# Kernel optimization log

Measured on AMD Instinct MI355X. Metric: run time of the kernel, lower is better.

## Reference

```python
import jax, jax.numpy as jnp
import numpy as np

N_SRC = 100000
N_DST = 100000
N_EDGES = 1600000
IN_FEATS = 256
HEADS = 4
D_OUT = 64
NEG_SLOPE = 0.2


def setup_inputs() -> dict:
    key = jax.random.key(0)
    ks = jax.random.split(key, 7)
    return {
        "feat_src": jax.random.normal(ks[0], (N_SRC, IN_FEATS), dtype=jnp.float32),
        "feat_dst": jax.random.normal(ks[1], (N_DST, IN_FEATS), dtype=jnp.float32),
        "edge_src": jax.random.randint(ks[2], (N_EDGES,), 0, N_SRC, dtype=jnp.int32),
        "edge_dst": jax.random.randint(ks[3], (N_EDGES,), 0, N_DST, dtype=jnp.int32),
        "W": jax.random.normal(ks[4], (IN_FEATS, HEADS * D_OUT), dtype=jnp.float32) * 0.06,
        "attn_l": jax.random.normal(ks[5], (HEADS, D_OUT), dtype=jnp.float32) * 0.1,
        "attn_r": jax.random.normal(ks[6], (HEADS, D_OUT), dtype=jnp.float32) * 0.1,
    }


def reference(feat_src, feat_dst, edge_src, edge_dst, W, attn_l, attn_r):
    # fc projection (no bias), reshape to [N, H, D]
    fsrc = (feat_src @ W).reshape(-1, HEADS, D_OUT)
    fdst = (feat_dst @ W).reshape(-1, HEADS, D_OUT)
    # per-node attention logits: el [N_src, H], er [N_dst, H]
    el = jnp.einsum('nhd,hd->nh', fsrc, attn_l)
    er = jnp.einsum('nhd,hd->nh', fdst, attn_r)
    # per-edge logit = leaky_relu(el[src] + er[dst]); original uses raw exp (no max-sub)
    e = el[edge_src] + er[edge_dst]                          # [E, H]
    e = jnp.where(e >= 0, e, NEG_SLOPE * e)
    s = jnp.exp(e)                                           # [E, H]
    # edge softmax denominator: segment sum over dst nodes
    out_sum = jax.ops.segment_sum(s, edge_dst, num_segments=N_DST)  # [N_dst, H]
    a = s / out_sum[edge_dst]                                # [E, H]
    # weighted neighbor aggregation: m = ft[src] * a, summed per dst
    m = fsrc[edge_src] * a[:, :, None]                       # [E, H, D]
    rst = jax.ops.segment_sum(m, edge_dst, num_segments=N_DST)      # [N_dst, H, D]
    return rst
```

## Files before the change

kernel.cpp:

```cpp
#include <hip/hip_runtime.h>
#include <hip/hip_bf16.h>
#include <math.h>

#define N_SRC   100000
#define N_DST   100000
#define N_EDGES 1600000
#define IN_F    256
#define HEADS   4
#define D_OUT   64
#define NHD     256
#define NEG_SLOPE 0.2f

typedef __attribute__((ext_vector_type(8))) short          bf16x8;
typedef __attribute__((ext_vector_type(8))) unsigned short u16x8;
typedef __attribute__((ext_vector_type(4))) float          f32x4;

__device__ inline void split_bf16(float x, unsigned short& h, unsigned short& l) {
    unsigned u = __float_as_uint(x);
    unsigned uh = u + (0x7fffu + ((u >> 16) & 1u));
    h = (unsigned short)(uh >> 16);
    float hf = __uint_as_float(uh & 0xffff0000u);
    float r = x - hf;
    unsigned ur = __float_as_uint(r);
    l = (unsigned short)((ur + (0x7fffu + ((ur >> 16) & 1u))) >> 16);
}

__global__ void k_wr(const float* __restrict__ W, const float* __restrict__ ar,
                     float* __restrict__ wr) {
    __shared__ float a[NHD];
    int t = threadIdx.x;
    a[t] = ar[t];
    __syncthreads();
    float s[HEADS] = {0.f, 0.f, 0.f, 0.f};
    for (int h = 0; h < HEADS; ++h) {
        float acc = 0.f;
        #pragma unroll 8
        for (int d = 0; d < D_OUT; ++d)
            acc += W[t * NHD + h * D_OUT + d] * a[h * D_OUT + d];
        s[h] = acc;
    }
    *(float4*)&wr[t * 4] = make_float4(s[0], s[1], s[2], s[3]);
}

__global__ void k_wcast(const float* __restrict__ W,
                        unsigned short* __restrict__ Wht,
                        unsigned short* __restrict__ Wlt) {
    int n = blockIdx.x;
    int k = threadIdx.x;
    float x = W[k * NHD + n];
    unsigned short h, l;
    split_bf16(x, h, l);
    Wht[n * IN_F + k] = h;
    Wlt[n * IN_F + k] = l;
}

__global__ __launch_bounds__(256) void k_er(const float* __restrict__ fdst,
                                            const float* __restrict__ wr,
                                            float* __restrict__ er) {
    __shared__ float4 wrs[256];
    int t = threadIdx.x;
    wrs[t] = ((const float4*)wr)[t];
    __syncthreads();
    int node = blockIdx.x * 4 + (t >> 6);
    int lane = t & 63;
    float4 f = *(const float4*)&fdst[(size_t)node * IN_F + lane * 4];
    float4 w0 = wrs[lane * 4 + 0], w1 = wrs[lane * 4 + 1];
    float4 w2 = wrs[lane * 4 + 2], w3 = wrs[lane * 4 + 3];
    float px = f.x * w0.x + f.y * w1.x + f.z * w2.x + f.w * w3.x;
    float py = f.x * w0.y + f.y * w1.y + f.z * w2.y + f.w * w3.y;
    float pz = f.x * w0.z + f.y * w1.z + f.z * w2.z + f.w * w3.z;
    float pw = f.x * w0.w + f.y * w1.w + f.z * w2.w + f.w * w3.w;
    #pragma unroll
    for (int m = 1; m < 64; m <<= 1) {
        px += __shfl_xor(px, m);
        py += __shfl_xor(py, m);
        pz += __shfl_xor(pz, m);
        pw += __shfl_xor(pw, m);
    }
    if (lane == 0)
        *(float4*)&er[node * 4] = make_float4(px, py, pz, pw);
}

#define GBM 128
#define GBK 32
__global__ __launch_bounds__(512, 2) void k_gemm_mfma(
        const float* __restrict__ A, const unsigned short* __restrict__ Bht,
        const unsigned short* __restrict__ Blt, const float* __restrict__ al_g,
        float* __restrict__ C, float* __restrict__ el) {
    __shared__ __align__(16) unsigned short Ah[GBM][GBK], Al[GBM][GBK];
    __shared__ __align__(16) unsigned short Bh[NHD][GBK], Bl[NHD][GBK];
    const int t = threadIdx.x;
    const int m0 = blockIdx.x * GBM;
    const int wid = t >> 6, lane = t & 63;
    const int wm = wid >> 2, wn = wid & 3;
    const int fr = lane & 15, fq = lane >> 4;
    const int kb = fq * 8;

    f32x4 acc[4][4];
    #pragma unroll
    for (int m = 0; m < 4; ++m)
        #pragma unroll
        for (int n = 0; n < 4; ++n)
            acc[m][n] = (f32x4){0.f, 0.f, 0.f, 0.f};

    const int ar = t >> 2, ac = (t & 3) * 8;
    const bool avalid = (m0 + ar) < N_SRC;
    const float* aptr = A + (size_t)(m0 + ar) * IN_F + ac;
    const int bn = t >> 1, bk = (t & 1) * 16;

    for (int k0 = 0; k0 < IN_F; k0 += GBK) {
        float4 v0 = make_float4(0.f, 0.f, 0.f, 0.f), v1 = v0;
        if (avalid) {
            v0 = *(const float4*)(aptr + k0);
            v1 = *(const float4*)(aptr + k0 + 4);
        }
        u16x8 bh0 = *(const u16x8*)(Bht + (size_t)bn * IN_F + k0 + bk);
        u16x8 bh1 = *(const u16x8*)(Bht + (size_t)bn * IN_F + k0 + bk + 8);
        u16x8 bl0 = *(const u16x8*)(Blt + (size_t)bn * IN_F + k0 + bk);
        u16x8 bl1 = *(const u16x8*)(Blt + (size_t)bn * IN_F + k0 + bk + 8);
        float xs[8] = {v0.x, v0.y, v0.z, v0.w, v1.x, v1.y, v1.z, v1.w};
        u16x8 hv, lv;
        #pragma unroll
        for (int j = 0; j < 8; ++j) {
            unsigned short hh, ll;
            split_bf16(xs[j], hh, ll);
            hv[j] = hh; lv[j] = ll;
        }
        __syncthreads();
        *(u16x8*)&Ah[ar][ac] = hv;
        *(u16x8*)&Al[ar][ac] = lv;
        *(u16x8*)&Bh[bn][bk]     = bh0;
        *(u16x8*)&Bh[bn][bk + 8] = bh1;
        *(u16x8*)&Bl[bn][bk]     = bl0;
        *(u16x8*)&Bl[bn][bk + 8] = bl1;
        __syncthreads();
        bf16x8 afh[4], afl[4], bfh[4], bfl[4];
        #pragma unroll
        for (int m = 0; m < 4; ++m) {
            afh[m] = *(const bf16x8*)&Ah[wm * 64 + m * 16 + fr][kb];
            afl[m] = *(const bf16x8*)&Al[wm * 64 + m * 16 + fr][kb];
        }
        #pragma unroll
        for (int n = 0; n < 4; ++n) {
            bfh[n] = *(const bf16x8*)&Bh[wn * 64 + n * 16 + fr][kb];
            bfl[n] = *(const bf16x8*)&Bl[wn * 64 + n * 16 + fr][kb];
        }
        #pragma unroll
        for (int m = 0; m < 4; ++m)
            #pragma unroll
            for (int n = 0; n < 4; ++n) {
                acc[m][n] = __builtin_amdgcn_mfma_f32_16x16x32_bf16(afh[m], bfh[n], acc[m][n], 0, 0, 0);
                acc[m][n] = __builtin_amdgcn_mfma_f32_16x16x32_bf16(afh[m], bfl[n], acc[m][n], 0, 0, 0);
                acc[m][n] = __builtin_amdgcn_mfma_f32_16x16x32_bf16(afl[m], bfh[n], acc[m][n], 0, 0, 0);
            }
    }

    float alw[4];
    #pragma unroll
    for (int n = 0; n < 4; ++n) alw[n] = al_g[wn * 64 + n * 16 + fr];
    #pragma unroll
    for (int m = 0; m < 4; ++m) {
        int rbase = m0 + wm * 64 + m * 16 + fq * 4;
        float elp[4] = {0.f, 0.f, 0.f, 0.f};
        #pragma unroll
        for (int n = 0; n < 4; ++n) {
            f32x4 a = acc[m][n];
            int col = wn * 64 + n * 16 + fr;
            float w = alw[n];
            elp[0] += a[0] * w; elp[1] += a[1] * w;
            elp[2] += a[2] * w; elp[3] += a[3] * w;
            #pragma unroll
            for (int j = 0; j < 4; ++j)
                if (rbase + j < N_SRC)
                    C[(size_t)(rbase + j) * NHD + col] = a[j];
        }
        #pragma unroll
        for (int j = 0; j < 4; ++j) {
            float s = elp[j];
            s += __shfl_xor(s, 1); s += __shfl_xor(s, 2);
            s += __shfl_xor(s, 4); s += __shfl_xor(s, 8);
            if (fr == 0 && rbase + j < N_SRC)
                el[(rbase + j) * HEADS + wn] = s;
        }
    }
}

__global__ void k_hist(const int* __restrict__ edst, int* __restrict__ deg) {
    int e = blockIdx.x * 256 + threadIdx.x;
    if (e < N_EDGES) atomicAdd(&deg[edst[e]], 1);
}

#define SCAN_B 1024
__global__ __launch_bounds__(SCAN_B) void k_scanA(const int* __restrict__ deg,
                                                  int* __restrict__ off,
                                                  int* __restrict__ bsum) {
    int t = threadIdx.x, b = blockIdx.x;
    int i = b * SCAN_B + t;
    int v = (i < N_DST) ? deg[i] : 0;
    int incl = v;
    int lane = t & 63, w = t >> 6;
    #pragma unroll
    for (int d = 1; d < 64; d <<= 1) {
        int u = __shfl_up(incl, d);
        if (lane >= d) incl += u;
    }
    __shared__ int ws[16];
    if (lane == 63) ws[w] = incl;
    __syncthreads();
    if (t == 0) {
        int run = 0;
        for (int j = 0; j < 16; ++j) { int x = ws[j]; ws[j] = run; run += x; }
        bsum[b] = run;
    }
    __syncthreads();
    if (i < N_DST) off[i] = incl - v + ws[w];
}

__global__ void k_scanB(int* __restrict__ bsum, int nb) {
    if (threadIdx.x == 0 && blockIdx.x == 0) {
        int run = 0;
        for (int j = 0; j < nb; ++j) { int x = bsum[j]; bsum[j] = run; run += x; }
    }
}

__global__ __launch_bounds__(SCAN_B) void k_scanC(int* __restrict__ off,
                                                  const int* __restrict__ bsum) {
    int t = threadIdx.x, b = blockIdx.x;
    int i = b * SCAN_B + t;
    if (i < N_DST) off[i] += bsum[b];
    if (i == 0) off[N_DST] = N_EDGES;
}

__global__ void k_scatter(const int* __restrict__ esrc, const int* __restrict__ edst,
                          const float* __restrict__ el, const float* __restrict__ er,
                          const int* __restrict__ off, int* __restrict__ cursor,
                          int* __restrict__ ssrc, float4* __restrict__ ss) {
    int e = blockIdx.x * 256 + threadIdx.x;
    if (e >= N_EDGES) return;
    int src = esrc[e], dst = edst[e];
    float4 l4 = *(const float4*)&el[src * 4];
    float4 r4 = *(const float4*)&er[dst * 4];
    float ex = l4.x + r4.x, ey = l4.y + r4.y, ez = l4.z + r4.z, ew = l4.w + r4.w;
    ex = (ex >= 0.f) ? ex : NEG_SLOPE * ex;
    ey = (ey >= 0.f) ? ey : NEG_SLOPE * ey;
    ez = (ez >= 0.f) ? ez : NEG_SLOPE * ez;
    ew = (ew >= 0.f) ? ew : NEG_SLOPE * ew;
    float4 s = make_float4(expf(ex), expf(ey), expf(ez), expf(ew));
    int pos = off[dst] + atomicAdd(&cursor[dst], 1);
    ssrc[pos] = src;
    ss[pos] = s;
}

__global__ __launch_bounds__(256) void k_agg(const int* __restrict__ off,
                                             const int* __restrict__ ssrc,
                                             const float* __restrict__ ss,
                                             const float* __restrict__ fsrc,
                                             float* __restrict__ out) {
    int b = blockIdx.x;
    int t = threadIdx.x;
    int s0 = off[b], s1 = off[b + 1];
    __shared__ float inv_den[HEADS];
    if (t < 64) {
        int h = t & 3;
        float p = 0.f;
        for (int i = s0 + (t >> 2); i < s1; i += 16)
            p += ss[(size_t)i * 4 + h];
        #pragma unroll
        for (int m = 4; m < 64; m <<= 1) p += __shfl_xor(p, m);
        if (t < 4) inv_den[t] = (p > 0.f) ? (1.0f / p) : 0.f;
    }
    __syncthreads();
    int h = t >> 6;
    float idh = inv_den[h];
    float acc = 0.f;
    int i = s0;
    int n4 = s0 + ((s1 - s0) & ~3);
    for (; i < n4; i += 4) {
        int sA = ssrc[i + 0], sB = ssrc[i + 1];
        int sC = ssrc[i + 2], sD = ssrc[i + 3];
        float aA = ss[(size_t)(i + 0) * 4 + h];
        float aB = ss[(size_t)(i + 1) * 4 + h];
        float aC = ss[(size_t)(i + 2) * 4 + h];
        float aD = ss[(size_t)(i + 3) * 4 + h];
        float fA = fsrc[(size_t)sA * NHD + t];
        float fB = fsrc[(size_t)sB * NHD + t];
        float fC = fsrc[(size_t)sC * NHD + t];
        float fD = fsrc[(size_t)sD * NHD + t];
        acc += aA * fA;
        acc += aB * fB;
        acc += aC * fC;
        acc += aD * fD;
    }
    for (; i < s1; ++i) {
        int src = ssrc[i];
        float a = ss[(size_t)i * 4 + h];
        acc += a * fsrc[(size_t)src * NHD + t];
    }
    out[(size_t)b * NHD + t] = acc * idh;
}

extern "C" void kernel_launch(void* const* d_in, const int* in_sizes, int n_in,
                              void* d_out, int out_size, void* d_ws, size_t ws_size,
                              hipStream_t stream) {
    const float* feat_src = (const float*)d_in[0];
    const float* feat_dst = (const float*)d_in[1];
    const int*   edge_src = (const int*)d_in[2];
    const int*   edge_dst = (const int*)d_in[3];
    const float* W        = (const float*)d_in[4];
    const float* attn_l   = (const float*)d_in[5];
    const float* attn_r   = (const float*)d_in[6];
    float* out = (float*)d_out;

    char* base = (char*)d_ws;
    float* fsrc     = (float*)(base);
    float* sorted_s = (float*)(base + 102400000);
    unsigned short* Wht = (unsigned short*)(base + 102400000);
    unsigned short* Wlt = (unsigned short*)(base + 102400000 + 131072);
    float* el       = (float*)(base + 128000000);
    float* er       = (float*)(base + 129600000);
    float* wr       = (float*)(base + 131200000);
    int*   deg      = (int*)  (base + 131204096);
    int*   off      = (int*)  (base + 131604096);
    int*   cursor   = (int*)  (base + 132004112);
    int*   bsum     = (int*)  (base + 132404112);
    int*   ssrc     = (int*)  (base + 132404624);

    hipMemsetAsync(deg, 0, N_DST * sizeof(int), stream);
    hipMemsetAsync(cursor, 0, N_DST * sizeof(int), stream);

    k_wr<<<1, 256, 0, stream>>>(W, attn_r, wr);
    k_wcast<<<256, 256, 0, stream>>>(W, Wht, Wlt);
    k_er<<<N_DST / 4, 256, 0, stream>>>(feat_dst, wr, er);
    int gblocks = (N_SRC + GBM - 1) / GBM;
    k_gemm_mfma<<<gblocks, 512, 0, stream>>>(feat_src, Wht, Wlt, attn_l, fsrc, el);
    k_hist<<<(N_EDGES + 255) / 256, 256, 0, stream>>>(edge_dst, deg);
    int nb = (N_DST + SCAN_B - 1) / SCAN_B;
    k_scanA<<<nb, SCAN_B, 0, stream>>>(deg, off, bsum);
    k_scanB<<<1, 64, 0, stream>>>(bsum, nb);
    k_scanC<<<nb, SCAN_B, 0, stream>>>(off, bsum);
    k_scatter<<<(N_EDGES + 255) / 256, 256, 0, stream>>>(
        edge_src, edge_dst, el, er, off, cursor, ssrc, (float4*)sorted_s);
    k_agg<<<N_DST, 256, 0, stream>>>(off, ssrc, sorted_s, fsrc, out);
}
```

Baseline: 735.4 us.

## Split aggregation edges across warps with float4 row loads and LDS reduction

```diff
diff --git a/kernel.cpp b/kernel.cpp
--- a/kernel.cpp
+++ b/kernel.cpp
@@ -259,44 +259,49 @@
     int b = blockIdx.x;
     int t = threadIdx.x;
     int s0 = off[b], s1 = off[b + 1];
+    int w = t >> 6, lane = t & 63;
+    int h = lane >> 4;
+    int col = lane << 2;
+
     __shared__ float inv_den[HEADS];
+    __shared__ float red[4][NHD];
+
     if (t < 64) {
-        int h = t & 3;
+        int hh = t & 3;
         float p = 0.f;
         for (int i = s0 + (t >> 2); i < s1; i += 16)
-            p += ss[(size_t)i * 4 + h];
+            p += ss[(size_t)i * 4 + hh];
         #pragma unroll
         for (int m = 4; m < 64; m <<= 1) p += __shfl_xor(p, m);
         if (t < 4) inv_den[t] = (p > 0.f) ? (1.0f / p) : 0.f;
     }
-    __syncthreads();
-    int h = t >> 6;
-    float idh = inv_den[h];
-    float acc = 0.f;
-    int i = s0;
-    int n4 = s0 + ((s1 - s0) & ~3);
-    for (; i < n4; i += 4) {
-        int sA = ssrc[i + 0], sB = ssrc[i + 1];
-        int sC = ssrc[i + 2], sD = ssrc[i + 3];
-        float aA = ss[(size_t)(i + 0) * 4 + h];
-        float aB = ss[(size_t)(i + 1) * 4 + h];
-        float aC = ss[(size_t)(i + 2) * 4 + h];
-        float aD = ss[(size_t)(i + 3) * 4 + h];
-        float fA = fsrc[(size_t)sA * NHD + t];
-        float fB = fsrc[(size_t)sB * NHD + t];
-        float fC = fsrc[(size_t)sC * NHD + t];
-        float fD = fsrc[(size_t)sD * NHD + t];
-        acc += aA * fA;
-        acc += aB * fB;
-        acc += aC * fC;
-        acc += aD * fD;
-    }
-    for (; i < s1; ++i) {
-        int src = ssrc[i];
-        float a = ss[(size_t)i * 4 + h];
-        acc += a * fsrc[(size_t)src * NHD + t];
-    }
-    out[(size_t)b * NHD + t] = acc * idh;
+
+    float4 acc = make_float4(0.f, 0.f, 0.f, 0.f);
+    int i = s0 + w;
+    for (; i + 4 < s1; i += 8) {
+        int   srcA = ssrc[i];
+        int   srcB = ssrc[i + 4];
+        float aA = ss[(size_t)i * 4 + h];
+        float aB = ss[(size_t)(i + 4) * 4 + h];
+        float4 fA = *(const float4*)&fsrc[(size_t)srcA * NHD + col];
+        float4 fB = *(const float4*)&fsrc[(size_t)srcB * NHD + col];
+        acc.x += aA * fA.x; acc.y += aA * fA.y;
+        acc.z += aA * fA.z; acc.w += aA * fA.w;
+        acc.x += aB * fB.x; acc.y += aB * fB.y;
+        acc.z += aB * fB.z; acc.w += aB * fB.w;
+    }
+    if (i < s1) {
+        int   src = ssrc[i];
+        float a   = ss[(size_t)i * 4 + h];
+        float4 f  = *(const float4*)&fsrc[(size_t)src * NHD + col];
+        acc.x += a * f.x; acc.y += a * f.y;
+        acc.z += a * f.z; acc.w += a * f.w;
+    }
+    *(float4*)&red[w][col] = acc;
+    __syncthreads();
+
+    float r = red[0][t] + red[1][t] + red[2][t] + red[3][t];
+    out[(size_t)b * NHD + t] = r * inv_den[t >> 6];
 }
 
 extern "C" void kernel_launch(void* const* d_in, const int* in_sizes, int n_in,
```

Result: no change. 726.4 us (-1.2%).
